# Kernel optimization log

Hardware: AMD Instinct MI355X
Metric: run time of the kernel (lower is better)

Reference implementation:

```python
import jax, jax.numpy as jnp
import numpy as np

U, I, D = 100000, 200000, 64   # users, items, emb_size
N = U + I                      # total nodes
NNZ = 6400000                  # adjacency non-zeros
B = 4096                       # batch of (user,item) pairs
L = 3                          # n_layers


def setup_inputs() -> dict:
    key = jax.random.key(0)
    ks = jax.random.split(key, 11)
    s = 1.0 / np.sqrt(D)  # xavier-ish scale
    return {
        "user_emb_online": jax.random.normal(ks[0], (U, D), jnp.float32) * s,
        "item_emb_online": jax.random.normal(ks[1], (I, D), jnp.float32) * s,
        "user_emb_target": jax.random.normal(ks[2], (U, D), jnp.float32) * s,
        "item_emb_target": jax.random.normal(ks[3], (I, D), jnp.float32) * s,
        # normalized adjacency values (positive, roughly 1/deg scale)
        "adj_val": jax.random.uniform(ks[4], (NNZ,), jnp.float32) * (1.0 / 16.0),
        "pred_w": jax.random.normal(ks[5], (D, D), jnp.float32) * s,
        "pred_b": jnp.zeros((D,), jnp.float32),
        "adj_row": jax.random.randint(ks[6], (NNZ,), 0, N, dtype=jnp.int32),
        "adj_col": jax.random.randint(ks[7], (NNZ,), 0, N, dtype=jnp.int32),
        "user_idx": jax.random.randint(ks[8], (B,), 0, U, dtype=jnp.int32),
        "item_idx": jax.random.randint(ks[9], (B,), 0, I, dtype=jnp.int32),
    }


def _spmm(row, col, val, x):
    # sparse [N,N] @ dense [N,D] via gather + segment-sum
    return jax.ops.segment_sum(val[:, None] * x[col], row, num_segments=N)


def _lgcn_encode(user_emb, item_emb, row, col, val):
    ego = jnp.concatenate([user_emb, item_emb], axis=0)  # [N, D]
    acc = ego
    x = ego
    for _ in range(L):
        x = _spmm(row, col, val, x)
        acc = acc + x
    all_emb = acc / (L + 1)  # mean over stacked layer outputs
    return all_emb[:U], all_emb[U:]


def reference(user_emb_online, item_emb_online, user_emb_target, item_emb_target,
              adj_val, pred_w, pred_b, adj_row, adj_col, user_idx, item_idx):
    u_on_all, i_on_all = _lgcn_encode(user_emb_online, item_emb_online, adj_row, adj_col, adj_val)
    u_tg_all, i_tg_all = _lgcn_encode(user_emb_target, item_emb_target, adj_row, adj_col, adj_val)
    u_online = u_on_all[user_idx]   # [B, D]
    i_online = i_on_all[item_idx]
    u_target = u_tg_all[user_idx]
    i_target = i_tg_all[item_idx]
    u_pred = u_online @ pred_w.T + pred_b  # nn.Linear
    i_pred = i_online @ pred_w.T + pred_b
    return (u_pred, u_target, i_pred, i_target)
```

## Files before the change

### kernel.cpp

```cpp
#include <hip/hip_runtime.h>
#include <hip/hip_bf16.h>
#include <stdint.h>

#define U_N   100000
#define I_N   200000
#define NN    300000
#define DD    64
#define NNZ_N 6400000
#define BB    4096
#define CHUNK 4096
#define NB    ((NN + CHUNK - 1) / CHUNK)
#define NBK   74
#define EPB   4096
#define NSB   1184
#define SUBCAP 6656
#define BKCAP  94208
#define BKBLK  23
#define LBLK   48000
#define P1B   ((NNZ_N + EPB - 1) / EPB)
#define PACKB ((NN * 16) / 256)
#define ACCB  ((2 * BB * 32) / 256)

typedef unsigned short u16;
typedef unsigned int   u32;
typedef float vf2 __attribute__((ext_vector_type(2)));

__device__ __forceinline__ u16 f2bf(float f) {
    u32 u = __float_as_uint(f);
    u32 r = (u + 0x7FFFu + ((u >> 16) & 1u)) >> 16;
    return (u16)r;
}


#if __has_builtin(__builtin_amdgcn_cvt_pk_f32_fp8) && __has_builtin(__builtin_amdgcn_cvt_pk_fp8_f32)
#define FP8_HW 1
#else
#define FP8_HW 0
#endif

__device__ __forceinline__ u32 enc1_fp8(float f) {
    float af = fabsf(f);
    u32 s = (__float_as_uint(f) >> 31) << 7;
    if (af >= 0.015625f) {
        u32 au = __float_as_uint(af);
        u32 r = au + 0x7FFFFu + ((au >> 20) & 1u);
        u32 e = (r >> 23) - 120u;
        u32 m = (r >> 20) & 7u;
        if (e > 15u) { e = 15u; m = 6u; }
        return s | (e << 3) | m;
    } else {
        u32 q = (u32)__float2int_rn(af * 512.0f);
        return s | q;
    }
}

__device__ __forceinline__ u32 pack4_fp8(float a, float b, float c, float d) {
#if FP8_HW
    u32 w = 0;
    w = (u32)__builtin_amdgcn_cvt_pk_fp8_f32(a, b, (int)w, false);
    w = (u32)__builtin_amdgcn_cvt_pk_fp8_f32(c, d, (int)w, true);
    return w;
#else
    return enc1_fp8(a) | (enc1_fp8(b) << 8) | (enc1_fp8(c) << 16) | (enc1_fp8(d) << 24);
#endif
}

__device__ __forceinline__ float dec1_fp8(u32 b) {
    u32 s = (b & 0x80u) << 24;
    u32 e = (b >> 3) & 15u;
    u32 m = b & 7u;
    float mag = e ? __uint_as_float(((e + 120u) << 23) | (m << 20))
                  : (float)m * 0.001953125f;
    return __uint_as_float(__float_as_uint(mag) | s);
}

__device__ __forceinline__ void dec_fp8x4(u32 w, float* f) {
#if FP8_HW
    vf2 lo = __builtin_amdgcn_cvt_pk_f32_fp8((int)w, false);
    vf2 hi = __builtin_amdgcn_cvt_pk_f32_fp8((int)w, true);
    f[0] = lo[0]; f[1] = lo[1]; f[2] = hi[0]; f[3] = hi[1];
#else
    f[0] = dec1_fp8(w & 255u); f[1] = dec1_fp8((w >> 8) & 255u);
    f[2] = dec1_fp8((w >> 16) & 255u); f[3] = dec1_fp8(w >> 24);
#endif
}


__global__ void setup_k(unsigned char* __restrict__ mark, unsigned char* __restrict__ bmark,
                        int* __restrict__ nlist, int* __restrict__ bkt_cursor) {
    int tid = blockIdx.x * 256 + threadIdx.x;
    if (tid < NN / 4) { ((u32*)mark)[tid] = 0; ((u32*)bmark)[tid] = 0; }
    if (tid < NBK) bkt_cursor[tid] = tid * BKCAP;
    if (tid == NN / 4) nlist[0] = 0;
}


__global__ __launch_bounds__(256) void fused1_k(const int* __restrict__ adj_row,
                                                const int* __restrict__ adj_col,
                                                const float* __restrict__ adj_val,
                                                int* __restrict__ bkt_cursor,
                                                int2* __restrict__ bed,
                                                const float* __restrict__ ue_on,
                                                const float* __restrict__ ie_on,
                                                const float* __restrict__ ue_tg,
                                                const float* __restrict__ ie_tg,
                                                unsigned char* __restrict__ x0f,
                                                const int* __restrict__ user_idx,
                                                const int* __restrict__ item_idx,
                                                float* __restrict__ out_acc) {
    __shared__ int lcnt[NBK];
    __shared__ int lbase[NBK];
    int bid = blockIdx.x;
    if (bid < P1B) {
        int base = bid * EPB;
        for (int i = threadIdx.x; i < NBK; i += 256) lcnt[i] = 0;
        __syncthreads();
        u32 pk[16]; float vv[16]; int bb[16]; int rk[16];
#pragma unroll
        for (int j = 0; j < 16; j++) {
            int e = base + j * 256 + threadIdx.x;
            bb[j] = -1;
            if (e < NNZ_N) {
                int r = adj_row[e];
                int c = adj_col[e];
                vv[j] = adj_val[e];
                int b = r >> 12;
                pk[j] = ((u32)(r & 4095) << 19) | (u32)c;
                bb[j] = b;
                rk[j] = atomicAdd(&lcnt[b], 1);
            }
        }
        __syncthreads();
        for (int i = threadIdx.x; i < NBK; i += 256)
            lbase[i] = atomicAdd(&bkt_cursor[i], lcnt[i]);
        __syncthreads();
#pragma unroll
        for (int j = 0; j < 16; j++) {
            if (bb[j] >= 0) {
                int p = lbase[bb[j]] + rk[j];
                bed[p] = make_int2((int)pk[j], __float_as_int(vv[j]));
            }
        }
        return;
    }
    bid -= P1B;
    if (bid < PACKB) {
        int tid = bid * 256 + threadIdx.x;
        int n = tid >> 4;
        int t = tid & 15;
        if (n >= NN) return;
        const float* src;
        int soff;
        if (t < 8) {
            soff = t * 8;
            src = (n < U_N) ? ue_on + (size_t)n * 64 : ie_on + (size_t)(n - U_N) * 64;
        } else {
            soff = (t - 8) * 8;
            src = (n < U_N) ? ue_tg + (size_t)n * 64 : ie_tg + (size_t)(n - U_N) * 64;
        }
        float4 f0 = *(const float4*)(src + soff);
        float4 f1 = *(const float4*)(src + soff + 4);
        uint2 o;
        o.x = pack4_fp8(f0.x, f0.y, f0.z, f0.w);
        o.y = pack4_fp8(f1.x, f1.y, f1.z, f1.w);
        *(uint2*)(x0f + (size_t)n * 128 + t * 8) = o;
        return;
    }
    bid -= PACKB;
    {
        int t = bid * 256 + threadIdx.x;
        int slot = t >> 5;
        int j = t & 31;
        if (slot >= 2 * BB) return;
        int node = (slot < BB) ? user_idx[slot] : U_N + item_idx[slot - BB];
        const float* src;
        int soff, doff;
        if (j < 16) {
            soff = j * 4; doff = j * 4;
            src = (node < U_N) ? ue_on + (size_t)node * 64 : ie_on + (size_t)(node - U_N) * 64;
        } else {
            soff = (j - 16) * 4; doff = 64 + (j - 16) * 4;
            src = (node < U_N) ? ue_tg + (size_t)node * 64 : ie_tg + (size_t)(node - U_N) * 64;
        }
        float4 f = *(const float4*)(src + soff);
        *(float4*)(out_acc + (size_t)slot * 128 + doff) = f;
    }
}


__global__ __launch_bounds__(1024) void fused2_k(const int* __restrict__ bkt_cursor,
                                                 const int2* __restrict__ bed,
                                                 int* __restrict__ cnt,
                                                 int* __restrict__ bsums,
                                                 int* __restrict__ row_ptr) {
    if (blockIdx.x < NBK) {
        __shared__ int h[4096];
        int b = blockIdx.x;
        int base = b * BKCAP;
        int e1 = bkt_cursor[b];
        for (int j = threadIdx.x; j < 4096; j += 1024) h[j] = 0;
        __syncthreads();
        for (int i = base + threadIdx.x; i < e1; i += 1024)
            atomicAdd(&h[(u32)bed[i].x >> 19], 1);
        __syncthreads();
        int rb = b << 12;
        for (int j = threadIdx.x; j < 4096; j += 1024) {
            int idx = rb + j;
            if (idx < NN) cnt[idx] = h[j];
        }
    } else {
        __shared__ int sh[128];
        int t = threadIdx.x;
        int v = 0;
        if (t < 128) {
            v = (t < NB) ? bkt_cursor[t] - t * BKCAP : 0;
            sh[t] = v;
        }
        __syncthreads();
        for (int o = 1; o < 128; o <<= 1) {
            int tmp = 0;
            if (t < 128 && t >= o) tmp = sh[t - o];
            __syncthreads();
            if (t < 128) sh[t] += tmp;
            __syncthreads();
        }
        if (t < NB) bsums[t] = sh[t] - v;
        if (t == 127) row_ptr[NN] = sh[127];
    }
}

__global__ void scan3_k(const int* __restrict__ cnt, const int* __restrict__ bsums,
                        int* __restrict__ row_ptr, int* __restrict__ sub_cursor) {
    __shared__ int tsum[256];
    int base = blockIdx.x * CHUNK;
    int loc[16];
    int s = 0;
#pragma unroll
    for (int j = 0; j < 16; j++) {
        int idx = base + threadIdx.x * 16 + j;
        int c = (idx < NN) ? cnt[idx] : 0;
        loc[j] = s;
        s += c;
    }
    tsum[threadIdx.x] = s;
    __syncthreads();
    int v = s;
    for (int o = 1; o < 256; o <<= 1) {
        int t = (threadIdx.x >= o) ? tsum[threadIdx.x - o] : 0;
        __syncthreads();
        tsum[threadIdx.x] += t;
        __syncthreads();
    }
    int texcl = tsum[threadIdx.x] - v;
    int boff = bsums[blockIdx.x];
#pragma unroll
    for (int j = 0; j < 16; j++) {
        int idx = base + threadIdx.x * 16 + j;
        if (idx < NN) {
            int val = boff + texcl + loc[j];
            row_ptr[idx] = val;
            if ((idx & 255) == 0) sub_cursor[idx >> 8] = val;
        }
    }
}


__global__ __launch_bounds__(256) void p2r_k(const int* __restrict__ bkt_cursor,
                                             const int2* __restrict__ bed,
                                             int* __restrict__ sub_cursor,
                                             int2* __restrict__ mid) {
    __shared__ int lcnt[16], lbase[16], sbase[16];
    __shared__ int2 stage[4096];
    int b = blockIdx.y;
    int e1 = bkt_cursor[b];
    int base = b * BKCAP + blockIdx.x * 4096;
    if (base >= e1) return;
    if (threadIdx.x < 16) lcnt[threadIdx.x] = 0;
    __syncthreads();
    u32 pk[16]; int dv[16]; int sb[16], rk[16];
#pragma unroll
    for (int j = 0; j < 16; j++) {
        int e = base + j * 256 + threadIdx.x;
        sb[j] = -1;
        if (e < e1) {
            int2 d = bed[e];
            pk[j] = (u32)d.x;
            dv[j] = d.y;
            int s = (int)((pk[j] >> 27) & 15u);
            sb[j] = s;
            rk[j] = atomicAdd(&lcnt[s], 1);
        }
    }
    __syncthreads();
    if (threadIdx.x == 0) {
        int acc = 0;
#pragma unroll
        for (int s = 0; s < 16; s++) { sbase[s] = acc; acc += lcnt[s]; }
    }
    if (threadIdx.x < 16)
        lbase[threadIdx.x] = atomicAdd(&sub_cursor[b * 16 + threadIdx.x], lcnt[threadIdx.x]);
    __syncthreads();
#pragma unroll
    for (int j = 0; j < 16; j++)
        if (sb[j] >= 0)
            stage[sbase[sb[j]] + rk[j]] = make_int2((int)pk[j], dv[j]);
    __syncthreads();
    for (int s = 0; s < 16; s++) {
        int c = lcnt[s], gb = lbase[s], lb = sbase[s];
        for (int i = threadIdx.x; i < c; i += 256)
            mid[gb + i] = stage[lb + i];
    }
}


__global__ __launch_bounds__(256) void p3_k(const int* __restrict__ row_ptr,
                                            const int2* __restrict__ mid,
                                            int2* __restrict__ edge_s) {
    __shared__ int rbase[256], rcur[256];
    __shared__ int2 stage[SUBCAP];
    int s = blockIdx.x;
    int r0 = s << 8;
    if (r0 >= NN) return;
    int r1 = min(r0 + 256, NN);
    int nr = r1 - r0;
    int ebase = row_ptr[r0];
    int eend  = row_ptr[r1];
    int cnt = eend - ebase;
    if (threadIdx.x < nr) {
        rbase[threadIdx.x] = row_ptr[r0 + threadIdx.x] - ebase;
        rcur[threadIdx.x] = 0;
    }
    __syncthreads();
    for (int i = threadIdx.x; i < cnt; i += 256) {
        int2 d = mid[ebase + i];
        u32 pk = (u32)d.x;
        int l = (int)((pk >> 19) & 255u);
        int pos = rbase[l] + atomicAdd(&rcur[l], 1);
        if (pos < SUBCAP) stage[pos] = make_int2((int)(pk & 0x7FFFFu), d.y);
    }
    __syncthreads();
    for (int i = threadIdx.x; i < cnt; i += 256) edge_s[ebase + i] = stage[i];
}


__global__ void mark_k(const int* __restrict__ row_ptr, const int2* __restrict__ edge_s,
                       const int* __restrict__ user_idx, const int* __restrict__ item_idx,
                       unsigned char* __restrict__ mark, unsigned char* __restrict__ bmark) {
    int wave = threadIdx.x >> 6;
    int lane = threadIdx.x & 63;
    int slot = blockIdx.x * 4 + wave;
    if (slot >= 2 * BB) return;
    int r = (slot < BB) ? user_idx[slot] : U_N + item_idx[slot - BB];
    if (lane == 0) { mark[r] = 1; bmark[r] = 1; }
    int e0 = row_ptr[r], e1 = row_ptr[r + 1];
    for (int e = e0 + lane; e < e1; e += 64) mark[edge_s[e].x] = 1;
}

__global__ void compact_k(const unsigned char* __restrict__ mark,
                          int* __restrict__ list2, int* __restrict__ nlist) {
    int i = blockIdx.x * 256 + threadIdx.x;
    int lane = threadIdx.x & 63;
    int m = (i < NN) ? (int)mark[i] : 0;
    unsigned long long b = __ballot(m != 0);
    int pre = __popcll(b & ((1ull << lane) - 1ull));
    int tot = __popcll(b);
    int base = 0;
    if (lane == 0 && tot) base = atomicAdd(nlist, tot);
    base = __shfl(base, 0);
    if (m) list2[base + pre] = i;
}


struct acc8 { float a[8]; };

__device__ __forceinline__ void red8(acc8& A) {
#pragma unroll
    for (int k = 0; k < 8; k++) {
        A.a[k] += __shfl_xor(A.a[k], 16);
        A.a[k] += __shfl_xor(A.a[k], 32);
    }
}

__device__ __forceinline__ void rg8_core(const int2* __restrict__ edge_s,
                                         const unsigned char* __restrict__ xf,
                                         int t, int g, int e0, int e1, acc8& A) {
#pragma unroll
    for (int k = 0; k < 8; k++) A.a[k] = 0.f;
    const unsigned char* xt = xf + t * 8;
    int d = e1 - e0;

    int2 ed[8];
    uint2 pv[8];
#pragma unroll
    for (int q = 0; q < 8; q++) { ed[q] = make_int2(0, 0); pv[q] = make_uint2(0u, 0u); }
#pragma unroll
    for (int q = 0; q < 8; q++) {
        int j = g + 4 * q;
        if (j < d) ed[q] = edge_s[e0 + j];
    }
#pragma unroll
    for (int q = 0; q < 8; q++) {
        int j = g + 4 * q;
        if (j < d) pv[q] = *(const uint2*)(xt + (size_t)((u32)ed[q].x * 128u));
    }
#pragma unroll
    for (int q = 0; q < 8; q++) {
        float v = __int_as_float(ed[q].y);
        float f[8];
        dec_fp8x4(pv[q].x, f);
        dec_fp8x4(pv[q].y, f + 4);
#pragma unroll
        for (int k = 0; k < 8; k++) A.a[k] += v * f[k];
    }
    for (int e = e0 + 32 + g * 4; e < e1; e += 16) {
        int m = e1 - e;
#pragma unroll
        for (int k = 0; k < 4; k++) {
            if (k < m) {
                int2 dd = edge_s[e + k];
                float v = __int_as_float(dd.y);
                uint2 p = *(const uint2*)(xt + (size_t)((u32)dd.x * 128u));
                float f[8];
                dec_fp8x4(p.x, f);
                dec_fp8x4(p.y, f + 4);
#pragma unroll
                for (int q = 0; q < 8; q++) A.a[q] += v * f[q];
            }
        }
    }
    red8(A);
}

__global__ __launch_bounds__(256) void spmm1_k(const int* __restrict__ row_ptr,
                                               const int2* __restrict__ edge_s,
                                               const unsigned char* __restrict__ x0f,
                                               const unsigned char* __restrict__ bmark,
                                               u16* __restrict__ y,
                                               unsigned char* __restrict__ yf) {
    int lane = threadIdx.x & 63;
    int t = lane & 15, g = lane >> 4;
    int r = blockIdx.x * 4 + (threadIdx.x >> 6);
    if (r >= NN) return;
    acc8 A;
    rg8_core(edge_s, x0f, t, g, row_ptr[r], row_ptr[r + 1], A);
    if (g == 0) {
        uint2 of;
        of.x = pack4_fp8(A.a[0], A.a[1], A.a[2], A.a[3]);
        of.y = pack4_fp8(A.a[4], A.a[5], A.a[6], A.a[7]);
        *(uint2*)(yf + (size_t)r * 128 + t * 8) = of;
        if (bmark[r]) {
            uint4 o;
            o.x = ((u32)f2bf(A.a[1]) << 16) | (u32)f2bf(A.a[0]);
            o.y = ((u32)f2bf(A.a[3]) << 16) | (u32)f2bf(A.a[2]);
            o.z = ((u32)f2bf(A.a[5]) << 16) | (u32)f2bf(A.a[4]);
            o.w = ((u32)f2bf(A.a[7]) << 16) | (u32)f2bf(A.a[6]);
            *(uint4*)(y + (size_t)r * 128 + t * 8) = o;
        }
    }
}

__device__ __forceinline__ void rg16_core(const int2* __restrict__ edge_s,
                                          const u16* __restrict__ x,
                                          int t, int g, int e0, int e1, acc8& A) {
#pragma unroll
    for (int k = 0; k < 8; k++) A.a[k] = 0.f;
    const u16* xt = x + t * 8;
    int d = e1 - e0;

    int2 ed[8];
    uint4 pv[8];
#pragma unroll
    for (int q = 0; q < 8; q++) { ed[q] = make_int2(0, 0); pv[q] = make_uint4(0u, 0u, 0u, 0u); }
#pragma unroll
    for (int q = 0; q < 8; q++) {
        int j = g + 4 * q;
        if (j < d) ed[q] = edge_s[e0 + j];
    }
#pragma unroll
    for (int q = 0; q < 8; q++) {
        int j = g + 4 * q;
        if (j < d) pv[q] = *(const uint4*)(xt + (size_t)(u32)ed[q].x * 128);
    }
#pragma unroll
    for (int q = 0; q < 8; q++) {
        float v = __int_as_float(ed[q].y);
        A.a[0] += v * __uint_as_float(pv[q].x << 16);
        A.a[1] += v * __uint_as_float(pv[q].x & 0xFFFF0000u);
        A.a[2] += v * __uint_as_float(pv[q].y << 16);
        A.a[3] += v * __uint_as_float(pv[q].y & 0xFFFF0000u);
        A.a[4] += v * __uint_as_float(pv[q].z << 16);
        A.a[5] += v * __uint_as_float(pv[q].z & 0xFFFF0000u);
        A.a[6] += v * __uint_as_float(pv[q].w << 16);
        A.a[7] += v * __uint_as_float(pv[q].w & 0xFFFF0000u);
    }
    for (int e = e0 + 32 + g * 4; e < e1; e += 16) {
        int m = e1 - e;
#pragma unroll
        for (int k = 0; k < 4; k++) {
            if (k < m) {
                int2 dd = edge_s[e + k];
                float v = __int_as_float(dd.y);
                uint4 p = *(const uint4*)(xt + (size_t)(u32)dd.x * 128);
                A.a[0] += v * __uint_as_float(p.x << 16);
                A.a[1] += v * __uint_as_float(p.x & 0xFFFF0000u);
                A.a[2] += v * __uint_as_float(p.y << 16);
                A.a[3] += v * __uint_as_float(p.y & 0xFFFF0000u);
                A.a[4] += v * __uint_as_float(p.z << 16);
                A.a[5] += v * __uint_as_float(p.z & 0xFFFF0000u);
                A.a[6] += v * __uint_as_float(p.w << 16);
                A.a[7] += v * __uint_as_float(p.w & 0xFFFF0000u);
            }
        }
    }
    red8(A);
}

__global__ __launch_bounds__(256) void spmm_list_k(const int* __restrict__ row_ptr,
                                                   const int2* __restrict__ edge_s,
                                                   const unsigned char* __restrict__ x1f,
                                                   u16* __restrict__ y,
                                                   const int* __restrict__ list2,
                                                   const int* __restrict__ nlist) {
    int lane = threadIdx.x & 63;
    int t = lane & 15, g = lane >> 4;
    int slot = blockIdx.x * 4 + (threadIdx.x >> 6);
    if (slot >= *nlist) return;
    int r = list2[slot];
    acc8 A;
    rg8_core(edge_s, x1f, t, g, row_ptr[r], row_ptr[r + 1], A);
    if (g == 0) {
        uint4 o;
        o.x = ((u32)f2bf(A.a[1]) << 16) | (u32)f2bf(A.a[0]);
        o.y = ((u32)f2bf(A.a[3]) << 16) | (u32)f2bf(A.a[2]);
        o.z = ((u32)f2bf(A.a[5]) << 16) | (u32)f2bf(A.a[4]);
        o.w = ((u32)f2bf(A.a[7]) << 16) | (u32)f2bf(A.a[6]);
        *(uint4*)(y + (size_t)r * 128 + t * 8) = o;
    }
}

__global__ __launch_bounds__(256) void spmm_last_k(const int* __restrict__ row_ptr,
                                                   const int2* __restrict__ edge_s,
                                                   const u16* __restrict__ x,
                                                   const int* __restrict__ user_idx,
                                                   const int* __restrict__ item_idx,
                                                   float* __restrict__ out_acc) {
    int lane = threadIdx.x & 63;
    int t = lane & 15, g = lane >> 4;
    int slot = blockIdx.x * 4 + (threadIdx.x >> 6);
    if (slot >= 2 * BB) return;
    int r = (slot < BB) ? user_idx[slot] : U_N + item_idx[slot - BB];
    acc8 A;
    rg16_core(edge_s, x, t, g, row_ptr[r], row_ptr[r + 1], A);
    if (g == 0) {
        uint4 p = *(const uint4*)(x + (size_t)r * 128 + t * 8);
        A.a[0] += __uint_as_float(p.x << 16);
        A.a[1] += __uint_as_float(p.x & 0xFFFF0000u);
        A.a[2] += __uint_as_float(p.y << 16);
        A.a[3] += __uint_as_float(p.y & 0xFFFF0000u);
        A.a[4] += __uint_as_float(p.z << 16);
        A.a[5] += __uint_as_float(p.z & 0xFFFF0000u);
        A.a[6] += __uint_as_float(p.w << 16);
        A.a[7] += __uint_as_float(p.w & 0xFFFF0000u);
        float4* p0 = (float4*)(out_acc + (size_t)slot * 128 + t * 8);
        float4 c0 = p0[0], c1 = p0[1];
        c0.x += A.a[0]; c0.y += A.a[1]; c0.z += A.a[2]; c0.w += A.a[3];
        c1.x += A.a[4]; c1.y += A.a[5]; c1.z += A.a[6]; c1.w += A.a[7];
        p0[0] = c0; p0[1] = c1;
    }
}


__global__ void gadd_k(const int* __restrict__ user_idx, const int* __restrict__ item_idx,
                       const u16* __restrict__ x, float* __restrict__ out_acc) {
    int t = blockIdx.x * blockDim.x + threadIdx.x;
    int slot = t >> 6;
    int l = t & 63;
    if (slot >= 2 * BB) return;
    int node = (slot < BB) ? user_idx[slot] : U_N + item_idx[slot - BB];
    u32 p = *(const u32*)(x + (size_t)node * 128 + (l << 1));
    float fx = __uint_as_float(p << 16);
    float fy = __uint_as_float(p & 0xFFFF0000u);
    float2* q = (float2*)(out_acc + (size_t)slot * 128) + l;
    float2 cur = *q;
    cur.x += fx; cur.y += fy;
    *q = cur;
}


__global__ __launch_bounds__(256) void pred_k(const float* __restrict__ out_acc,
                                              const float* __restrict__ W,
                                              const float* __restrict__ bias,
                                              float* __restrict__ out) {
    __shared__ float wld[64 * 65];
    __shared__ float uld[4 * 64];
    int j = threadIdx.x & 63;
    int rl = threadIdx.x >> 6;
    for (int i = threadIdx.x; i < 4096; i += 256) {
        int jj = i >> 6, kk = i & 63;
        wld[kk * 65 + jj] = W[i];
    }
    int slot = blockIdx.x * 4 + rl;
    uld[rl * 64 + j] = out_acc[(size_t)slot * 128 + j] * 0.25f;
    float tv = out_acc[(size_t)slot * 128 + 64 + j] * 0.25f;
    size_t tdst = (slot < BB) ? (size_t)BB * 64 + (size_t)slot * 64 + j
                              : (size_t)3 * BB * 64 + (size_t)(slot - BB) * 64 + j;
    out[tdst] = tv;
    __syncthreads();
    float acc = bias[j];
#pragma unroll
    for (int k = 0; k < 64; k++) acc += uld[rl * 64 + k] * wld[k * 65 + j];
    size_t dst = (slot < BB) ? (size_t)slot * 64 + j
                             : (size_t)2 * BB * 64 + (size_t)(slot - BB) * 64 + j;
    out[dst] = acc;
}


extern "C" void kernel_launch(void* const* d_in, const int* in_sizes, int n_in,
                              void* d_out, int out_size, void* d_ws, size_t ws_size,
                              hipStream_t stream) {
    const float* ue_on = (const float*)d_in[0];
    const float* ie_on = (const float*)d_in[1];
    const float* ue_tg = (const float*)d_in[2];
    const float* ie_tg = (const float*)d_in[3];
    const float* adj_val = (const float*)d_in[4];
    const float* pred_w = (const float*)d_in[5];
    const float* pred_b = (const float*)d_in[6];
    const int* adj_row = (const int*)d_in[7];
    const int* adj_col = (const int*)d_in[8];
    const int* user_idx = (const int*)d_in[9];
    const int* item_idx = (const int*)d_in[10];
    float* out = (float*)d_out;

    char* ws = (char*)d_ws;
    size_t off = 0;
    auto alloc = [&](size_t bytes) -> char* {
        char* p = ws + off;
        off = (off + bytes + 255) & ~(size_t)255;
        return p;
    };
    int*   cnt        = (int*)alloc((size_t)NN * 4);
    int*   row_ptr    = (int*)alloc((size_t)(NN + 1) * 4);
    int*   bsums      = (int*)alloc(256 * 4);
    int*   bkt_cursor = (int*)alloc(256 * 4);
    int*   sub_cursor = (int*)alloc((size_t)NSB * 4);
    unsigned char* mark = (unsigned char*)alloc((size_t)NN);
    unsigned char* bmark = (unsigned char*)alloc((size_t)NN);
    int*   list2      = (int*)alloc((size_t)NN * 4);
    int*   nlist      = (int*)alloc(256 * 4);
    int2*  edge_s     = (int2*)alloc((size_t)NNZ_N * 8);
    u16*   x_a        = (u16*)alloc((size_t)NN * 128 * 2);
    u16*   x_b        = (u16*)alloc((size_t)NN * 128 * 2);
    float* out_acc    = (float*)alloc((size_t)2 * BB * 128 * 4);

    unsigned char* x0f = (unsigned char*)x_a;
    unsigned char* x1f = (unsigned char*)x_a + (size_t)NN * 128;
    int2*  bed  = (int2*)x_b;
    int2*  mid  = edge_s;

    (void)n_in; (void)in_sizes; (void)out_size; (void)ws_size;

    setup_k<<<294, 256, 0, stream>>>(mark, bmark, nlist, bkt_cursor);
    fused1_k<<<P1B + PACKB + ACCB, 256, 0, stream>>>(adj_row, adj_col, adj_val,
                                                     bkt_cursor, bed,
                                                     ue_on, ie_on, ue_tg, ie_tg, x0f,
                                                     user_idx, item_idx, out_acc);
    fused2_k<<<NBK + 1, 1024, 0, stream>>>(bkt_cursor, bed, cnt, bsums, row_ptr);
    scan3_k<<<NB, 256, 0, stream>>>(cnt, bsums, row_ptr, sub_cursor);
    p2r_k<<<dim3(BKBLK, NBK), 256, 0, stream>>>(bkt_cursor, bed, sub_cursor, mid);
    p3_k<<<NSB, 256, 0, stream>>>(row_ptr, mid, edge_s);

    mark_k<<<(2 * BB) / 4, 256, 0, stream>>>(row_ptr, edge_s, user_idx, item_idx, mark, bmark);
    compact_k<<<(NN + 255) / 256, 256, 0, stream>>>(mark, list2, nlist);

    spmm1_k<<<NN / 4, 256, 0, stream>>>(row_ptr, edge_s, x0f, bmark, x_b, x1f);
    gadd_k<<<(2 * BB * 64) / 256, 256, 0, stream>>>(user_idx, item_idx, x_b, out_acc);
    spmm_list_k<<<LBLK, 256, 0, stream>>>(row_ptr, edge_s, x1f, x_b, list2, nlist);
    spmm_last_k<<<(2 * BB) / 4, 256, 0, stream>>>(row_ptr, edge_s, x_b, user_idx, item_idx, out_acc);

    pred_k<<<(2 * BB) / 4, 256, 0, stream>>>(out_acc, pred_w, pred_b, out);
}
```

Measured before the change: 726.1 us.

## Fuse neighbor marking into bucketing pass and vectorize histogram/scatter loops

```diff
diff --git a/kernel.cpp b/kernel.cpp
--- a/kernel.cpp
+++ b/kernel.cpp
@@ -95,11 +95,23 @@
 }
 
 
+__global__ void bmark_k(const int* __restrict__ user_idx, const int* __restrict__ item_idx,
+                        unsigned char* __restrict__ mark, unsigned char* __restrict__ bmark) {
+    int slot = blockIdx.x * 256 + threadIdx.x;
+    if (slot >= 2 * BB) return;
+    int r = (slot < BB) ? user_idx[slot] : U_N + item_idx[slot - BB];
+    bmark[r] = 1;
+    mark[r] = 1;
+}
+
+
 __global__ __launch_bounds__(256) void fused1_k(const int* __restrict__ adj_row,
                                                 const int* __restrict__ adj_col,
                                                 const float* __restrict__ adj_val,
                                                 int* __restrict__ bkt_cursor,
                                                 int2* __restrict__ bed,
+                                                const unsigned char* __restrict__ bmark,
+                                                unsigned char* __restrict__ mark,
                                                 const float* __restrict__ ue_on,
                                                 const float* __restrict__ ie_on,
                                                 const float* __restrict__ ue_tg,
@@ -128,6 +140,7 @@
                 pk[j] = ((u32)(r & 4095) << 19) | (u32)c;
                 bb[j] = b;
                 rk[j] = atomicAdd(&lcnt[b], 1);
+                if (bmark[r]) mark[c] = 1;
             }
         }
         __syncthreads();
@@ -198,10 +211,28 @@
         int b = blockIdx.x;
         int base = b * BKCAP;
         int e1 = bkt_cursor[b];
+        int len = e1 - base;
         for (int j = threadIdx.x; j < 4096; j += 1024) h[j] = 0;
         __syncthreads();
-        for (int i = base + threadIdx.x; i < e1; i += 1024)
-            atomicAdd(&h[(u32)bed[i].x >> 19], 1);
+        const int4* bed4 = (const int4*)(bed + base);
+        int np = len >> 1;
+        int t = threadIdx.x;
+        int i = t;
+        for (; i + 3072 < np; i += 4096) {
+            int4 a  = bed4[i];
+            int4 b2 = bed4[i + 1024];
+            int4 c2 = bed4[i + 2048];
+            int4 d2 = bed4[i + 3072];
+            atomicAdd(&h[(u32)a.x  >> 19], 1); atomicAdd(&h[(u32)a.z  >> 19], 1);
+            atomicAdd(&h[(u32)b2.x >> 19], 1); atomicAdd(&h[(u32)b2.z >> 19], 1);
+            atomicAdd(&h[(u32)c2.x >> 19], 1); atomicAdd(&h[(u32)c2.z >> 19], 1);
+            atomicAdd(&h[(u32)d2.x >> 19], 1); atomicAdd(&h[(u32)d2.z >> 19], 1);
+        }
+        for (; i < np; i += 1024) {
+            int4 a = bed4[i];
+            atomicAdd(&h[(u32)a.x >> 19], 1); atomicAdd(&h[(u32)a.z >> 19], 1);
+        }
+        if (t == 0 && (len & 1)) atomicAdd(&h[(u32)bed[e1 - 1].x >> 19], 1);
         __syncthreads();
         int rb = b << 12;
         for (int j = threadIdx.x; j < 4096; j += 1024) {
@@ -331,30 +362,35 @@
         rcur[threadIdx.x] = 0;
     }
     __syncthreads();
-    for (int i = threadIdx.x; i < cnt; i += 256) {
+    int i = threadIdx.x;
+    for (; i + 768 < cnt; i += 1024) {
+        int2 d0 = mid[ebase + i];
+        int2 d1 = mid[ebase + i + 256];
+        int2 d2 = mid[ebase + i + 512];
+        int2 d3 = mid[ebase + i + 768];
+        int l0 = (int)(((u32)d0.x >> 19) & 255u);
+        int p0 = rbase[l0] + atomicAdd(&rcur[l0], 1);
+        if (p0 < SUBCAP) stage[p0] = make_int2(d0.x & 0x7FFFF, d0.y);
+        int l1 = (int)(((u32)d1.x >> 19) & 255u);
+        int p1 = rbase[l1] + atomicAdd(&rcur[l1], 1);
+        if (p1 < SUBCAP) stage[p1] = make_int2(d1.x & 0x7FFFF, d1.y);
+        int l2 = (int)(((u32)d2.x >> 19) & 255u);
+        int p2 = rbase[l2] + atomicAdd(&rcur[l2], 1);
+        if (p2 < SUBCAP) stage[p2] = make_int2(d2.x & 0x7FFFF, d2.y);
+        int l3 = (int)(((u32)d3.x >> 19) & 255u);
+        int p3 = rbase[l3] + atomicAdd(&rcur[l3], 1);
+        if (p3 < SUBCAP) stage[p3] = make_int2(d3.x & 0x7FFFF, d3.y);
+    }
+    for (; i < cnt; i += 256) {
         int2 d = mid[ebase + i];
-        u32 pk = (u32)d.x;
-        int l = (int)((pk >> 19) & 255u);
+        int l = (int)(((u32)d.x >> 19) & 255u);
         int pos = rbase[l] + atomicAdd(&rcur[l], 1);
-        if (pos < SUBCAP) stage[pos] = make_int2((int)(pk & 0x7FFFFu), d.y);
+        if (pos < SUBCAP) stage[pos] = make_int2(d.x & 0x7FFFF, d.y);
     }
     __syncthreads();
-    for (int i = threadIdx.x; i < cnt; i += 256) edge_s[ebase + i] = stage[i];
-}
-
-
-__global__ void mark_k(const int* __restrict__ row_ptr, const int2* __restrict__ edge_s,
-                       const int* __restrict__ user_idx, const int* __restrict__ item_idx,
-                       unsigned char* __restrict__ mark, unsigned char* __restrict__ bmark) {
-    int wave = threadIdx.x >> 6;
-    int lane = threadIdx.x & 63;
-    int slot = blockIdx.x * 4 + wave;
-    if (slot >= 2 * BB) return;
-    int r = (slot < BB) ? user_idx[slot] : U_N + item_idx[slot - BB];
-    if (lane == 0) { mark[r] = 1; bmark[r] = 1; }
-    int e0 = row_ptr[r], e1 = row_ptr[r + 1];
-    for (int e = e0 + lane; e < e1; e += 64) mark[edge_s[e].x] = 1;
-}
+    for (int j = threadIdx.x; j < cnt; j += 256) edge_s[ebase + j] = stage[j];
+}
+
 
 __global__ void compact_k(const unsigned char* __restrict__ mark,
                           int* __restrict__ list2, int* __restrict__ nlist) {
@@ -660,18 +696,18 @@
     (void)n_in; (void)in_sizes; (void)out_size; (void)ws_size;
 
     setup_k<<<294, 256, 0, stream>>>(mark, bmark, nlist, bkt_cursor);
+    bmark_k<<<(2 * BB) / 256, 256, 0, stream>>>(user_idx, item_idx, mark, bmark);
     fused1_k<<<P1B + PACKB + ACCB, 256, 0, stream>>>(adj_row, adj_col, adj_val,
-                                                     bkt_cursor, bed,
+                                                     bkt_cursor, bed, bmark, mark,
                                                      ue_on, ie_on, ue_tg, ie_tg, x0f,
                                                      user_idx, item_idx, out_acc);
+    compact_k<<<(NN + 255) / 256, 256, 0, stream>>>(mark, list2, nlist);
+
     fused2_k<<<NBK + 1, 1024, 0, stream>>>(bkt_cursor, bed, cnt, bsums, row_ptr);
     scan3_k<<<NB, 256, 0, stream>>>(cnt, bsums, row_ptr, sub_cursor);
     p2r_k<<<dim3(BKBLK, NBK), 256, 0, stream>>>(bkt_cursor, bed, sub_cursor, mid);
     p3_k<<<NSB, 256, 0, stream>>>(row_ptr, mid, edge_s);
 
-    mark_k<<<(2 * BB) / 4, 256, 0, stream>>>(row_ptr, edge_s, user_idx, item_idx, mark, bmark);
-    compact_k<<<(NN + 255) / 256, 256, 0, stream>>>(mark, list2, nlist);
-
     spmm1_k<<<NN / 4, 256, 0, stream>>>(row_ptr, edge_s, x0f, bmark, x_b, x1f);
     gadd_k<<<(2 * BB * 64) / 256, 256, 0, stream>>>(user_idx, item_idx, x_b, out_acc);
     spmm_list_k<<<LBLK, 256, 0, stream>>>(row_ptr, edge_s, x1f, x_b, list2, nlist);
```

Result: faster. 710.8 us (-2.1%).
